# Kernel optimization log

Measured on AMD Instinct MI355X. Metric: run time of the kernel, lower is better.

Reference implementation:

```python
import jax, jax.numpy as jnp
import numpy as np
from jax import lax

IN_CH = 256
NF = 128
B, H, W = 8, 256, 256


def _bn_relu(y, s, b):
    # inference-mode BatchNorm folded into per-channel affine, then ReLU
    return jax.nn.relu(y * s[None, :, None, None] + b[None, :, None, None])


def _upsample_bilinear_ac(x, scale):
    # bilinear upsample, align_corners=True (matches torch nn.Upsample)
    b, c, h, w = x.shape
    Ho, Wo = h * scale, w * scale
    ys = jnp.arange(Ho, dtype=x.dtype) * ((h - 1) / (Ho - 1))
    xs = jnp.arange(Wo, dtype=x.dtype) * ((w - 1) / (Wo - 1))
    y0 = jnp.floor(ys).astype(jnp.int32)
    x0 = jnp.floor(xs).astype(jnp.int32)
    y1 = jnp.minimum(y0 + 1, h - 1)
    x1 = jnp.minimum(x0 + 1, w - 1)
    wy = (ys - y0.astype(x.dtype))[None, None, :, None]
    wx = (xs - x0.astype(x.dtype))[None, None, None, :]
    # interpolate rows then columns
    top = x[:, :, y0, :] * (1 - wy) + x[:, :, y1, :] * wy      # [b,c,Ho,w]
    out = top[:, :, :, x0] * (1 - wx) + top[:, :, :, x1] * wx  # [b,c,Ho,Wo]
    return out


def setup_inputs() -> dict:
    key = jax.random.key(0)
    ks = jax.random.split(key, 6)
    inp = {
        "x": jax.random.normal(ks[0], (B, 64, H, W), dtype=jnp.float32),
        "w1": jax.random.normal(ks[1], (IN_CH, 64, 8, 8), dtype=jnp.float32) * 0.02,
        "bn1_s": jnp.ones((IN_CH,), jnp.float32),
        "bn1_b": jnp.zeros((IN_CH,), jnp.float32),
        "w_fai": jax.random.normal(ks[2], (NF, IN_CH), dtype=jnp.float32) * 0.05,
        "bnf_s": jnp.ones((NF,), jnp.float32),
        "bnf_b": jnp.zeros((NF,), jnp.float32),
        "w_sit": jax.random.normal(ks[3], (NF, IN_CH), dtype=jnp.float32) * 0.05,
        "bns_s": jnp.ones((NF,), jnp.float32),
        "bns_b": jnp.zeros((NF,), jnp.float32),
        "w_gama": jax.random.normal(ks[4], (NF, IN_CH), dtype=jnp.float32) * 0.05,
        "bng_s": jnp.ones((NF,), jnp.float32),
        "bng_b": jnp.zeros((NF,), jnp.float32),
    }
    return inp


def reference(x, w1, bn1_s, bn1_b, w_fai, bnf_s, bnf_b, w_sit, bns_s, bns_b,
              w_gama, bng_s, bng_b):
    # conv1: 8x8 stride-8 conv, BN, ReLU  -> [B, IN_CH, h, w]
    y = lax.conv_general_dilated(x, w1, window_strides=(8, 8), padding="VALID",
                                 dimension_numbers=("NCHW", "OIHW", "NCHW"))
    y = _bn_relu(y, bn1_s, bn1_b)
    b, c, h, w = y.shape
    n = h * w
    # 1x1 conv projections (einsum), BN, ReLU
    fai = _bn_relu(jnp.einsum("bchw,oc->bohw", y, w_fai), bnf_s, bnf_b)
    sit = _bn_relu(jnp.einsum("bchw,oc->bohw", y, w_sit), bns_s, bns_b)
    gama = _bn_relu(jnp.einsum("bchw,oc->bohw", y, w_gama), bng_s, bng_b)
    fai = fai.reshape(b, NF, n)
    sit = sit.reshape(b, NF, n)
    gama = gama.reshape(b, NF, n)
    # non-local attention: sigmoid(fai^T sit) @ gama^T
    sf = jax.nn.sigmoid(jnp.einsum("bcn,bcm->bnm", fai, sit))  # [b, n, n]
    out = jnp.einsum("bnm,bcm->bcn", sf, gama)                  # [b, NF, n]
    out = out.reshape(b, NF, h, w)
    return _upsample_bilinear_ac(out, 8)
```

## Files before the change

kernel.cpp:

```cpp
#include <hip/hip_runtime.h>

typedef __attribute__((ext_vector_type(8))) short short8_t;
typedef __attribute__((ext_vector_type(4))) float float4_t;

__device__ __forceinline__ unsigned short f2bf(float f) {
    unsigned int u = __float_as_uint(f);
    return (unsigned short)((u + 0x7FFFu + ((u >> 16) & 1u)) >> 16);
}
__device__ __forceinline__ unsigned int pkbf(float a, float b) {
    return (unsigned int)f2bf(a) | ((unsigned int)f2bf(b) << 16);
}

__global__ __launch_bounds__(256, 1) void k_conv1(
    const float* __restrict__ x, const float* __restrict__ w1,
    const float* __restrict__ s1, const float* __restrict__ b1,
    unsigned short* __restrict__ y)
{
    __shared__ unsigned short At[128 * 40];
    __shared__ unsigned short Bt[64 * 40];
    const int tid = threadIdx.x;
    const int nt = blockIdx.x, mt = blockIdx.y;
    const int m0 = mt * 128, n0 = nt * 64;
    const int bi = m0 >> 10;
    const int oh0 = (m0 & 1023) >> 5;
    const int lane = tid & 63, wid = tid >> 6;
    const int wm = wid & 1, wn = wid >> 1;
    const int quad = lane >> 4, r16 = lane & 15;
    const int rA = tid >> 4, segA = tid & 15;
    const int ohl = rA >> 2, khl = rA & 3;
    float4_t acc[4][2] = {};

    for (int k0 = 0; k0 < 4096; k0 += 32) {
        const int ic = k0 >> 6;
        const int kh0 = (k0 >> 3) & 7;
        {
            const int xr = (oh0 + ohl) * 8 + kh0 + khl;
            const float* src = x + (((bi * 64 + ic) * 256 + xr) * 256 + segA * 16);
            const float4* s4 = (const float4*)src;
            float4 v0 = s4[0], v1 = s4[1], v2 = s4[2], v3 = s4[3];
            const int dst = (ohl * 32 + segA * 2) * 40 + khl * 8;
            int4 p0, p1;
            p0.x = pkbf(v0.x, v0.y); p0.y = pkbf(v0.z, v0.w);
            p0.z = pkbf(v1.x, v1.y); p0.w = pkbf(v1.z, v1.w);
            p1.x = pkbf(v2.x, v2.y); p1.y = pkbf(v2.z, v2.w);
            p1.z = pkbf(v3.x, v3.y); p1.w = pkbf(v3.z, v3.w);
            *(int4*)&At[dst] = p0;
            *(int4*)&At[dst + 40] = p1;
        }
        #pragma unroll
        for (int j = 0; j < 2; ++j) {
            const int id = j * 256 + tid;
            const int row = id >> 3, p = id & 7;
            float4 v = *(const float4*)(w1 + (n0 + row) * 4096 + k0 + p * 4);
            int2 wv; wv.x = pkbf(v.x, v.y); wv.y = pkbf(v.z, v.w);
            *(int2*)&Bt[row * 40 + p * 4] = wv;
        }
        __syncthreads();
        short8_t aF[4], bF[2];
        #pragma unroll
        for (int i = 0; i < 4; ++i)
            aF[i] = *(const short8_t*)&At[(wm * 64 + i * 16 + r16) * 40 + quad * 8];
        #pragma unroll
        for (int j = 0; j < 2; ++j)
            bF[j] = *(const short8_t*)&Bt[(wn * 32 + j * 16 + r16) * 40 + quad * 8];
        #pragma unroll
        for (int i = 0; i < 4; ++i)
            #pragma unroll
            for (int j = 0; j < 2; ++j)
                acc[i][j] = __builtin_amdgcn_mfma_f32_16x16x32_bf16(aF[i], bF[j], acc[i][j], 0, 0, 0);
        __syncthreads();
    }
    #pragma unroll
    for (int i = 0; i < 4; ++i) {
        const int mg = m0 + wm * 64 + i * 16 + quad * 4;
        #pragma unroll
        for (int j = 0; j < 2; ++j) {
            const int ng = n0 + wn * 32 + j * 16 + r16;
            const float sc = s1[ng], bc = b1[ng];
            #pragma unroll
            for (int r = 0; r < 4; ++r) {
                float v = fmaxf(acc[i][j][r] * sc + bc, 0.f);
                y[(mg + r) * 256 + ng] = f2bf(v);
            }
        }
    }
}

__global__ __launch_bounds__(256, 1) void k_proj(
    const unsigned short* __restrict__ y,
    const float* __restrict__ w_fai, const float* __restrict__ w_sit,
    const float* __restrict__ fs, const float* __restrict__ fb,
    const float* __restrict__ ss, const float* __restrict__ sb,
    unsigned short* __restrict__ P)
{
    __shared__ unsigned short At[128 * 40];
    __shared__ unsigned short Bt[64 * 40];
    const int tid = threadIdx.x;
    const int nt = blockIdx.x, mt = blockIdx.y;
    const int m0 = mt * 128, n0 = nt * 64;
    const float* wsrc = (n0 < 128) ? w_fai : w_sit;
    const float* scs  = (n0 < 128) ? fs : ss;
    const float* bcs  = (n0 < 128) ? fb : sb;
    const int noff = n0 & 127;
    const int lane = tid & 63, wid = tid >> 6;
    const int wm = wid & 1, wn = wid >> 1;
    const int quad = lane >> 4, r16 = lane & 15;
    float4_t acc[4][2] = {};

    for (int k0 = 0; k0 < 256; k0 += 32) {
        #pragma unroll
        for (int j = 0; j < 2; ++j) {
            const int id = j * 256 + tid;
            const int row = id >> 2, p = id & 3;
            int4 v = *(const int4*)(y + (m0 + row) * 256 + k0 + p * 8);
            *(int4*)&At[row * 40 + p * 8] = v;
        }
        #pragma unroll
        for (int j = 0; j < 2; ++j) {
            const int id = j * 256 + tid;
            const int row = id >> 3, p = id & 7;
            float4 v = *(const float4*)(wsrc + (noff + row) * 256 + k0 + p * 4);
            int2 wv; wv.x = pkbf(v.x, v.y); wv.y = pkbf(v.z, v.w);
            *(int2*)&Bt[row * 40 + p * 4] = wv;
        }
        __syncthreads();
        short8_t aF[4], bF[2];
        #pragma unroll
        for (int i = 0; i < 4; ++i)
            aF[i] = *(const short8_t*)&At[(wm * 64 + i * 16 + r16) * 40 + quad * 8];
        #pragma unroll
        for (int j = 0; j < 2; ++j)
            bF[j] = *(const short8_t*)&Bt[(wn * 32 + j * 16 + r16) * 40 + quad * 8];
        #pragma unroll
        for (int i = 0; i < 4; ++i)
            #pragma unroll
            for (int j = 0; j < 2; ++j)
                acc[i][j] = __builtin_amdgcn_mfma_f32_16x16x32_bf16(aF[i], bF[j], acc[i][j], 0, 0, 0);
        __syncthreads();
    }
    #pragma unroll
    for (int i = 0; i < 4; ++i) {
        const int mg = m0 + wm * 64 + i * 16 + quad * 4;
        #pragma unroll
        for (int j = 0; j < 2; ++j) {
            const int ng = n0 + wn * 32 + j * 16 + r16;
            const float sc = scs[ng & 127], bc = bcs[ng & 127];
            #pragma unroll
            for (int r = 0; r < 4; ++r) {
                float v = fmaxf(acc[i][j][r] * sc + bc, 0.f);
                P[(mg + r) * 256 + ng] = f2bf(v);
            }
        }
    }
}

__global__ __launch_bounds__(256, 1) void k_gama(
    const unsigned short* __restrict__ y, const float* __restrict__ wg,
    const float* __restrict__ gs, const float* __restrict__ gb,
    unsigned short* __restrict__ G)
{
    __shared__ unsigned short At[64 * 40];
    __shared__ unsigned short Bt[64 * 40];
    const int tid = threadIdx.x;
    const int nt = blockIdx.x, mt = blockIdx.y;
    const int m0 = mt * 64, n0 = nt * 64;
    const int lane = tid & 63, wid = tid >> 6;
    const int wm = wid & 1, wn = wid >> 1;
    const int quad = lane >> 4, r16 = lane & 15;
    float4_t acc[2][2] = {};

    for (int k0 = 0; k0 < 256; k0 += 32) {
        #pragma unroll
        for (int j = 0; j < 2; ++j) {
            const int id = j * 256 + tid;
            const int row = id >> 3, p = id & 7;
            float4 v = *(const float4*)(wg + (m0 + row) * 256 + k0 + p * 4);
            int2 wv; wv.x = pkbf(v.x, v.y); wv.y = pkbf(v.z, v.w);
            *(int2*)&At[row * 40 + p * 4] = wv;
        }
        {
            const int row = tid >> 2, p = tid & 3;
            int4 v = *(const int4*)(y + (n0 + row) * 256 + k0 + p * 8);
            *(int4*)&Bt[row * 40 + p * 8] = v;
        }
        __syncthreads();
        short8_t aF[2], bF[2];
        #pragma unroll
        for (int i = 0; i < 2; ++i)
            aF[i] = *(const short8_t*)&At[(wm * 32 + i * 16 + r16) * 40 + quad * 8];
        #pragma unroll
        for (int j = 0; j < 2; ++j)
            bF[j] = *(const short8_t*)&Bt[(wn * 32 + j * 16 + r16) * 40 + quad * 8];
        #pragma unroll
        for (int i = 0; i < 2; ++i)
            #pragma unroll
            for (int j = 0; j < 2; ++j)
                acc[i][j] = __builtin_amdgcn_mfma_f32_16x16x32_bf16(aF[i], bF[j], acc[i][j], 0, 0, 0);
        __syncthreads();
    }
    #pragma unroll
    for (int i = 0; i < 2; ++i) {
        const int cbase = m0 + wm * 32 + i * 16 + quad * 4;
        #pragma unroll
        for (int j = 0; j < 2; ++j) {
            const int ngg = n0 + wn * 32 + j * 16 + r16;
            const int nb = ngg >> 10, msp = ngg & 1023;
            #pragma unroll
            for (int r = 0; r < 4; ++r) {
                const int c = cbase + r;
                float v = fmaxf(acc[i][j][r] * gs[c] + gb[c], 0.f);
                G[(nb * 128 + c) * 1024 + msp] = f2bf(v);
            }
        }
    }
}

__global__ __launch_bounds__(256, 1) void k_logits(
    const unsigned short* __restrict__ P, unsigned short* __restrict__ sf)
{
    __shared__ unsigned short At[128 * 40];
    __shared__ unsigned short Bt[64 * 40];
    const int tid = threadIdx.x;
    const int nt = blockIdx.x, mt = blockIdx.y, b = blockIdx.z;
    const int m0 = mt * 128, n0 = nt * 64;
    const int base = b * 1024;
    const int lane = tid & 63, wid = tid >> 6;
    const int wm = wid & 1, wn = wid >> 1;
    const int quad = lane >> 4, r16 = lane & 15;
    float4_t acc[4][2] = {};

    for (int k0 = 0; k0 < 128; k0 += 32) {
        #pragma unroll
        for (int j = 0; j < 2; ++j) {
            const int id = j * 256 + tid;
            const int row = id >> 2, p = id & 3;
            int4 v = *(const int4*)(P + (base + m0 + row) * 256 + k0 + p * 8);
            *(int4*)&At[row * 40 + p * 8] = v;
        }
        {
            const int row = tid >> 2, p = tid & 3;
            int4 v = *(const int4*)(P + (base + n0 + row) * 256 + 128 + k0 + p * 8);
            *(int4*)&Bt[row * 40 + p * 8] = v;
        }
        __syncthreads();
        short8_t aF[4], bF[2];
        #pragma unroll
        for (int i = 0; i < 4; ++i)
            aF[i] = *(const short8_t*)&At[(wm * 64 + i * 16 + r16) * 40 + quad * 8];
        #pragma unroll
        for (int j = 0; j < 2; ++j)
            bF[j] = *(const short8_t*)&Bt[(wn * 32 + j * 16 + r16) * 40 + quad * 8];
        #pragma unroll
        for (int i = 0; i < 4; ++i)
            #pragma unroll
            for (int j = 0; j < 2; ++j)
                acc[i][j] = __builtin_amdgcn_mfma_f32_16x16x32_bf16(aF[i], bF[j], acc[i][j], 0, 0, 0);
        __syncthreads();
    }
    #pragma unroll
    for (int i = 0; i < 4; ++i) {
        const int mg = m0 + wm * 64 + i * 16 + quad * 4;
        #pragma unroll
        for (int j = 0; j < 2; ++j) {
            const int ng = n0 + wn * 32 + j * 16 + r16;
            #pragma unroll
            for (int r = 0; r < 4; ++r) {
                float v = 1.0f / (1.0f + expf(-acc[i][j][r]));
                sf[b * 1048576 + (mg + r) * 1024 + ng] = f2bf(v);
            }
        }
    }
}

__global__ __launch_bounds__(256, 1) void k_av(
    const unsigned short* __restrict__ sf, const unsigned short* __restrict__ G,
    float* __restrict__ O)
{
    __shared__ unsigned short At[64 * 40];
    __shared__ unsigned short Bt[64 * 40];
    const int tid = threadIdx.x;
    const int nt = blockIdx.x, mt = blockIdx.y, b = blockIdx.z;
    const int m0 = mt * 64, n0 = nt * 64;
    const int lane = tid & 63, wid = tid >> 6;
    const int wm = wid & 1, wn = wid >> 1;
    const int quad = lane >> 4, r16 = lane & 15;
    float4_t acc[2][2] = {};

    for (int k0 = 0; k0 < 1024; k0 += 32) {
        {
            const int row = tid >> 2, p = tid & 3;
            int4 v = *(const int4*)(sf + b * 1048576 + (m0 + row) * 1024 + k0 + p * 8);
            *(int4*)&At[row * 40 + p * 8] = v;
            int4 v2 = *(const int4*)(G + (b * 128 + n0 + row) * 1024 + k0 + p * 8);
            *(int4*)&Bt[row * 40 + p * 8] = v2;
        }
        __syncthreads();
        short8_t aF[2], bF[2];
        #pragma unroll
        for (int i = 0; i < 2; ++i)
            aF[i] = *(const short8_t*)&At[(wm * 32 + i * 16 + r16) * 40 + quad * 8];
        #pragma unroll
        for (int j = 0; j < 2; ++j)
            bF[j] = *(const short8_t*)&Bt[(wn * 32 + j * 16 + r16) * 40 + quad * 8];
        #pragma unroll
        for (int i = 0; i < 2; ++i)
            #pragma unroll
            for (int j = 0; j < 2; ++j)
                acc[i][j] = __builtin_amdgcn_mfma_f32_16x16x32_bf16(aF[i], bF[j], acc[i][j], 0, 0, 0);
        __syncthreads();
    }
    #pragma unroll
    for (int i = 0; i < 2; ++i) {
        const int mg = m0 + wm * 32 + i * 16 + quad * 4;
        #pragma unroll
        for (int j = 0; j < 2; ++j) {
            const int ng = n0 + wn * 32 + j * 16 + r16;
            #pragma unroll
            for (int r = 0; r < 4; ++r)
                O[b * 131072 + (mg + r) * 128 + ng] = acc[i][j][r];
        }
    }
}

__global__ __launch_bounds__(256, 1) void k_up(
    const float* __restrict__ O, float* __restrict__ out)
{
    __shared__ float l0[32 * 136];
    __shared__ float l1[32 * 136];
    const int tid = threadIdx.x;
    const int yb = blockIdx.x, b = blockIdx.y;
    const float sc = 31.0f / 255.0f;
    const float fy = yb * sc;
    const int y0 = (int)fy;
    const float wy = fy - (float)y0;
    const int y1 = min(y0 + 1, 31);
    const float4* r0 = (const float4*)(O + b * 131072 + y0 * 4096);
    const float4* r1 = (const float4*)(O + b * 131072 + y1 * 4096);
    #pragma unroll
    for (int j = 0; j < 4; ++j) {
        const int id = j * 256 + tid;
        const int xs = id >> 5, c4 = id & 31;
        *(float4*)(l0 + xs * 136 + c4 * 4) = r0[id];
        *(float4*)(l1 + xs * 136 + c4 * 4) = r1[id];
    }
    __syncthreads();
    const float fx = tid * sc;
    const int x0 = (int)fx;
    const float wx = fx - (float)x0;
    const int x1 = min(x0 + 1, 31);
    const float w00 = (1.f - wy) * (1.f - wx), w01 = (1.f - wy) * wx;
    const float w10 = wy * (1.f - wx), w11 = wy * wx;
    const float* a = l0 + x0 * 136;
    const float* bq = l0 + x1 * 136;
    const float* c = l1 + x0 * 136;
    const float* d = l1 + x1 * 136;
    float* op = out + b * 8388608 + yb * 256 + tid;
    #pragma unroll 4
    for (int ch = 0; ch < 128; ++ch)
        op[ch * 65536] = w00 * a[ch] + w01 * bq[ch] + w10 * c[ch] + w11 * d[ch];
}

extern "C" void kernel_launch(void* const* d_in, const int* in_sizes, int n_in,
                              void* d_out, int out_size, void* d_ws, size_t ws_size,
                              hipStream_t stream) {
    (void)in_sizes; (void)n_in; (void)out_size; (void)ws_size;
    const float* x      = (const float*)d_in[0];
    const float* w1     = (const float*)d_in[1];
    const float* bn1_s  = (const float*)d_in[2];
    const float* bn1_b  = (const float*)d_in[3];
    const float* w_fai  = (const float*)d_in[4];
    const float* bnf_s  = (const float*)d_in[5];
    const float* bnf_b  = (const float*)d_in[6];
    const float* w_sit  = (const float*)d_in[7];
    const float* bns_s  = (const float*)d_in[8];
    const float* bns_b  = (const float*)d_in[9];
    const float* w_gama = (const float*)d_in[10];
    const float* bng_s  = (const float*)d_in[11];
    const float* bng_b  = (const float*)d_in[12];
    float* out = (float*)d_out;

    char* ws = (char*)d_ws;
    unsigned short* y  = (unsigned short*)(ws);
    unsigned short* P  = (unsigned short*)(ws + 4u * 1024 * 1024);
    unsigned short* G  = (unsigned short*)(ws + 8u * 1024 * 1024);
    unsigned short* sf = (unsigned short*)(ws + 10u * 1024 * 1024);
    float*          O  = (float*)(ws + 26u * 1024 * 1024);

    k_conv1 <<<dim3(4, 64),    256, 0, stream>>>(x, w1, bn1_s, bn1_b, y);
    k_proj  <<<dim3(4, 64),    256, 0, stream>>>(y, w_fai, w_sit, bnf_s, bnf_b, bns_s, bns_b, P);
    k_gama  <<<dim3(128, 2),   256, 0, stream>>>(y, w_gama, bng_s, bng_b, G);
    k_logits<<<dim3(16, 8, 8), 256, 0, stream>>>(P, sf);
    k_av    <<<dim3(2, 16, 8), 256, 0, stream>>>(sf, G, O);
    k_up    <<<dim3(256, 8),   256, 0, stream>>>(O, out);
}
```

Baseline: 555.3 us.

## Split-K conv1 and attention-value GEMMs, fuse projections, prefetch conv tiles

Conv1 now covers all 256 output channels per block, splits K four ways across blocks, and prefetches the next tile into registers with a swizzled LDS layout. A new reduce kernel sums the partials and applies BN and ReLU. The three 1x1 projections are merged into one kernel. The attention-value GEMM is split-K by four, and the upsample kernel sums those partials as it loads. The aim is more blocks in flight for the under-filled GEMMs, at the cost of extra partial-sum traffic in global memory and one more launch.

```diff
diff --git a/kernel.cpp b/kernel.cpp
--- a/kernel.cpp
+++ b/kernel.cpp
@@ -11,177 +11,164 @@
     return (unsigned int)f2bf(a) | ((unsigned int)f2bf(b) << 16);
 }
 
-__global__ __launch_bounds__(256, 1) void k_conv1(
+__global__ __launch_bounds__(512, 2) void k_conv1(
     const float* __restrict__ x, const float* __restrict__ w1,
-    const float* __restrict__ s1, const float* __restrict__ b1,
-    unsigned short* __restrict__ y)
+    float* __restrict__ part)
 {
     __shared__ unsigned short At[128 * 40];
-    __shared__ unsigned short Bt[64 * 40];
+    __shared__ unsigned short Bt[256 * 40];
     const int tid = threadIdx.x;
-    const int nt = blockIdx.x, mt = blockIdx.y;
-    const int m0 = mt * 128, n0 = nt * 64;
-    const int bi = m0 >> 10;
-    const int oh0 = (m0 & 1023) >> 5;
+    const int mt = blockIdx.x, kc = blockIdx.y;
+    const int m0 = mt * 128;
+    const int bi = mt >> 3;
+    const int oh0 = (mt & 7) * 4;
     const int lane = tid & 63, wid = tid >> 6;
     const int wm = wid & 1, wn = wid >> 1;
     const int quad = lane >> 4, r16 = lane & 15;
-    const int rA = tid >> 4, segA = tid & 15;
+    const bool isA = tid < 256;
+    const int tA = tid & 255;
+    const int rA = tA >> 4, segA = tA & 15;
     const int ohl = rA >> 2, khl = rA & 3;
-    float4_t acc[4][2] = {};
-
-    for (int k0 = 0; k0 < 4096; k0 += 32) {
-        const int ic = k0 >> 6;
-        const int kh0 = (k0 >> 3) & 7;
-        {
-            const int xr = (oh0 + ohl) * 8 + kh0 + khl;
-            const float* src = x + (((bi * 64 + ic) * 256 + xr) * 256 + segA * 16);
-            const float4* s4 = (const float4*)src;
-            float4 v0 = s4[0], v1 = s4[1], v2 = s4[2], v3 = s4[3];
-            const int dst = (ohl * 32 + segA * 2) * 40 + khl * 8;
+    const int rowA = ohl * 32 + segA * 2;
+    const int koffA = (khl ^ (segA & 3)) * 8;
+    const int kbase = kc * 1024;
+    float4_t acc[4][4] = {};
+    float4 ra[4];
+    float4 rb[8];
+
+    if (isA) {
+        const int ic = kbase >> 6, kh0 = (kbase >> 3) & 7;
+        const int xr = (oh0 + ohl) * 8 + kh0 + khl;
+        const float4* s4 = (const float4*)(x + (((bi * 64 + ic) * 256 + xr) * 256 + segA * 16));
+        ra[0] = s4[0]; ra[1] = s4[1]; ra[2] = s4[2]; ra[3] = s4[3];
+    } else {
+        #pragma unroll
+        for (int l = 0; l < 8; ++l) {
+            const int slot = l * 256 + tA;
+            const int row = slot >> 3, p = slot & 7;
+            rb[l] = *(const float4*)(w1 + row * 4096 + kbase + p * 4);
+        }
+    }
+
+    for (int it = 0; it < 32; ++it) {
+        if (isA) {
             int4 p0, p1;
-            p0.x = pkbf(v0.x, v0.y); p0.y = pkbf(v0.z, v0.w);
-            p0.z = pkbf(v1.x, v1.y); p0.w = pkbf(v1.z, v1.w);
-            p1.x = pkbf(v2.x, v2.y); p1.y = pkbf(v2.z, v2.w);
-            p1.z = pkbf(v3.x, v3.y); p1.w = pkbf(v3.z, v3.w);
-            *(int4*)&At[dst] = p0;
-            *(int4*)&At[dst + 40] = p1;
-        }
-        #pragma unroll
-        for (int j = 0; j < 2; ++j) {
-            const int id = j * 256 + tid;
-            const int row = id >> 3, p = id & 7;
-            float4 v = *(const float4*)(w1 + (n0 + row) * 4096 + k0 + p * 4);
-            int2 wv; wv.x = pkbf(v.x, v.y); wv.y = pkbf(v.z, v.w);
-            *(int2*)&Bt[row * 40 + p * 4] = wv;
-        }
-        __syncthreads();
-        short8_t aF[4], bF[2];
+            p0.x = pkbf(ra[0].x, ra[0].y); p0.y = pkbf(ra[0].z, ra[0].w);
+            p0.z = pkbf(ra[1].x, ra[1].y); p0.w = pkbf(ra[1].z, ra[1].w);
+            p1.x = pkbf(ra[2].x, ra[2].y); p1.y = pkbf(ra[2].z, ra[2].w);
+            p1.z = pkbf(ra[3].x, ra[3].y); p1.w = pkbf(ra[3].z, ra[3].w);
+            *(int4*)&At[rowA * 40 + koffA] = p0;
+            *(int4*)&At[(rowA + 1) * 40 + koffA] = p1;
+        } else {
+            #pragma unroll
+            for (int l = 0; l < 8; ++l) {
+                const int slot = l * 256 + tA;
+                const int row = slot >> 3, p = slot & 7;
+                int2 wv; wv.x = pkbf(rb[l].x, rb[l].y); wv.y = pkbf(rb[l].z, rb[l].w);
+                *(int2*)&Bt[row * 40 + p * 4] = wv;
+            }
+        }
+        __syncthreads();
+        if (it + 1 < 32) {
+            const int k0 = kbase + (it + 1) * 32;
+            if (isA) {
+                const int ic = k0 >> 6, kh0 = (k0 >> 3) & 7;
+                const int xr = (oh0 + ohl) * 8 + kh0 + khl;
+                const float4* s4 = (const float4*)(x + (((bi * 64 + ic) * 256 + xr) * 256 + segA * 16));
+                ra[0] = s4[0]; ra[1] = s4[1]; ra[2] = s4[2]; ra[3] = s4[3];
+            } else {
+                #pragma unroll
+                for (int l = 0; l < 8; ++l) {
+                    const int slot = l * 256 + tA;
+                    const int row = slot >> 3, p = slot & 7;
+                    rb[l] = *(const float4*)(w1 + row * 4096 + k0 + p * 4);
+                }
+            }
+        }
+        short8_t aF[4], bF[4];
+        #pragma unroll
+        for (int i = 0; i < 4; ++i) {
+            const int R = wm * 64 + i * 16 + r16;
+            aF[i] = *(const short8_t*)&At[R * 40 + (quad ^ ((r16 >> 1) & 3)) * 8];
+        }
+        #pragma unroll
+        for (int j = 0; j < 4; ++j)
+            bF[j] = *(const short8_t*)&Bt[(wn * 64 + j * 16 + r16) * 40 + quad * 8];
         #pragma unroll
         for (int i = 0; i < 4; ++i)
-            aF[i] = *(const short8_t*)&At[(wm * 64 + i * 16 + r16) * 40 + quad * 8];
-        #pragma unroll
-        for (int j = 0; j < 2; ++j)
-            bF[j] = *(const short8_t*)&Bt[(wn * 32 + j * 16 + r16) * 40 + quad * 8];
-        #pragma unroll
-        for (int i = 0; i < 4; ++i)
-            #pragma unroll
-            for (int j = 0; j < 2; ++j)
+            #pragma unroll
+            for (int j = 0; j < 4; ++j)
                 acc[i][j] = __builtin_amdgcn_mfma_f32_16x16x32_bf16(aF[i], bF[j], acc[i][j], 0, 0, 0);
         __syncthreads();
     }
+    float* pp = part + ((size_t)kc << 21);
     #pragma unroll
     for (int i = 0; i < 4; ++i) {
         const int mg = m0 + wm * 64 + i * 16 + quad * 4;
         #pragma unroll
-        for (int j = 0; j < 2; ++j) {
-            const int ng = n0 + wn * 32 + j * 16 + r16;
-            const float sc = s1[ng], bc = b1[ng];
-            #pragma unroll
-            for (int r = 0; r < 4; ++r) {
-                float v = fmaxf(acc[i][j][r] * sc + bc, 0.f);
-                y[(mg + r) * 256 + ng] = f2bf(v);
-            }
-        }
-    }
-}
-
-__global__ __launch_bounds__(256, 1) void k_proj(
+        for (int j = 0; j < 4; ++j) {
+            const int ng = wn * 64 + j * 16 + r16;
+            #pragma unroll
+            for (int r = 0; r < 4; ++r)
+                pp[(mg + r) * 256 + ng] = acc[i][j][r];
+        }
+    }
+}
+
+__global__ __launch_bounds__(256, 4) void k_reduce(
+    const float* __restrict__ part, const float* __restrict__ s1,
+    const float* __restrict__ b1, unsigned short* __restrict__ y)
+{
+    const int id = blockIdx.x * 256 + threadIdx.x;
+    const int c4 = id & 63;
+    const float4* p = (const float4*)part + id;
+    float4 a = p[0], b = p[524288], c = p[1048576], d = p[1572864];
+    float4 s = ((const float4*)s1)[c4], bb = ((const float4*)b1)[c4];
+    float vx = fmaxf((a.x + b.x + c.x + d.x) * s.x + bb.x, 0.f);
+    float vy = fmaxf((a.y + b.y + c.y + d.y) * s.y + bb.y, 0.f);
+    float vz = fmaxf((a.z + b.z + c.z + d.z) * s.z + bb.z, 0.f);
+    float vw = fmaxf((a.w + b.w + c.w + d.w) * s.w + bb.w, 0.f);
+    int2 o; o.x = pkbf(vx, vy); o.y = pkbf(vz, vw);
+    ((int2*)y)[id] = o;
+}
+
+__global__ __launch_bounds__(256, 2) void k_proj3(
     const unsigned short* __restrict__ y,
     const float* __restrict__ w_fai, const float* __restrict__ w_sit,
+    const float* __restrict__ w_gama,
     const float* __restrict__ fs, const float* __restrict__ fb,
     const float* __restrict__ ss, const float* __restrict__ sb,
-    unsigned short* __restrict__ P)
-{
-    __shared__ unsigned short At[128 * 40];
-    __shared__ unsigned short Bt[64 * 40];
-    const int tid = threadIdx.x;
-    const int nt = blockIdx.x, mt = blockIdx.y;
-    const int m0 = mt * 128, n0 = nt * 64;
-    const float* wsrc = (n0 < 128) ? w_fai : w_sit;
-    const float* scs  = (n0 < 128) ? fs : ss;
-    const float* bcs  = (n0 < 128) ? fb : sb;
-    const int noff = n0 & 127;
-    const int lane = tid & 63, wid = tid >> 6;
-    const int wm = wid & 1, wn = wid >> 1;
-    const int quad = lane >> 4, r16 = lane & 15;
-    float4_t acc[4][2] = {};
-
-    for (int k0 = 0; k0 < 256; k0 += 32) {
-        #pragma unroll
-        for (int j = 0; j < 2; ++j) {
-            const int id = j * 256 + tid;
-            const int row = id >> 2, p = id & 3;
-            int4 v = *(const int4*)(y + (m0 + row) * 256 + k0 + p * 8);
-            *(int4*)&At[row * 40 + p * 8] = v;
-        }
-        #pragma unroll
-        for (int j = 0; j < 2; ++j) {
-            const int id = j * 256 + tid;
-            const int row = id >> 3, p = id & 7;
-            float4 v = *(const float4*)(wsrc + (noff + row) * 256 + k0 + p * 4);
-            int2 wv; wv.x = pkbf(v.x, v.y); wv.y = pkbf(v.z, v.w);
-            *(int2*)&Bt[row * 40 + p * 4] = wv;
-        }
-        __syncthreads();
-        short8_t aF[4], bF[2];
-        #pragma unroll
-        for (int i = 0; i < 4; ++i)
-            aF[i] = *(const short8_t*)&At[(wm * 64 + i * 16 + r16) * 40 + quad * 8];
-        #pragma unroll
-        for (int j = 0; j < 2; ++j)
-            bF[j] = *(const short8_t*)&Bt[(wn * 32 + j * 16 + r16) * 40 + quad * 8];
-        #pragma unroll
-        for (int i = 0; i < 4; ++i)
-            #pragma unroll
-            for (int j = 0; j < 2; ++j)
-                acc[i][j] = __builtin_amdgcn_mfma_f32_16x16x32_bf16(aF[i], bF[j], acc[i][j], 0, 0, 0);
-        __syncthreads();
-    }
-    #pragma unroll
-    for (int i = 0; i < 4; ++i) {
-        const int mg = m0 + wm * 64 + i * 16 + quad * 4;
-        #pragma unroll
-        for (int j = 0; j < 2; ++j) {
-            const int ng = n0 + wn * 32 + j * 16 + r16;
-            const float sc = scs[ng & 127], bc = bcs[ng & 127];
-            #pragma unroll
-            for (int r = 0; r < 4; ++r) {
-                float v = fmaxf(acc[i][j][r] * sc + bc, 0.f);
-                P[(mg + r) * 256 + ng] = f2bf(v);
-            }
-        }
-    }
-}
-
-__global__ __launch_bounds__(256, 1) void k_gama(
-    const unsigned short* __restrict__ y, const float* __restrict__ wg,
     const float* __restrict__ gs, const float* __restrict__ gb,
-    unsigned short* __restrict__ G)
+    unsigned short* __restrict__ P, unsigned short* __restrict__ G)
 {
     __shared__ unsigned short At[64 * 40];
     __shared__ unsigned short Bt[64 * 40];
     const int tid = threadIdx.x;
     const int nt = blockIdx.x, mt = blockIdx.y;
-    const int m0 = mt * 64, n0 = nt * 64;
+    const int m0 = mt * 64;
+    const float *W, *S, *Bb;
+    if (nt < 2)      { W = w_fai;  S = fs; Bb = fb; }
+    else if (nt < 4) { W = w_sit;  S = ss; Bb = sb; }
+    else             { W = w_gama; S = gs; Bb = gb; }
+    const int roff = (nt * 64) & 127;
     const int lane = tid & 63, wid = tid >> 6;
     const int wm = wid & 1, wn = wid >> 1;
     const int quad = lane >> 4, r16 = lane & 15;
     float4_t acc[2][2] = {};
 
     for (int k0 = 0; k0 < 256; k0 += 32) {
-        #pragma unroll
-        for (int j = 0; j < 2; ++j) {
-            const int id = j * 256 + tid;
-            const int row = id >> 3, p = id & 7;
-            float4 v = *(const float4*)(wg + (m0 + row) * 256 + k0 + p * 4);
+        {
+            const int row = tid >> 2, pp = tid & 3;
+            *(int4*)&At[row * 40 + pp * 8] =
+                *(const int4*)(y + (m0 + row) * 256 + k0 + pp * 8);
+        }
+        #pragma unroll
+        for (int l = 0; l < 2; ++l) {
+            const int slot = l * 256 + tid;
+            const int row = slot >> 3, pp = slot & 7;
+            float4 v = *(const float4*)(W + (roff + row) * 256 + k0 + pp * 4);
             int2 wv; wv.x = pkbf(v.x, v.y); wv.y = pkbf(v.z, v.w);
-            *(int2*)&At[row * 40 + p * 4] = wv;
-        }
-        {
-            const int row = tid >> 2, p = tid & 3;
-            int4 v = *(const int4*)(y + (n0 + row) * 256 + k0 + p * 8);
-            *(int4*)&Bt[row * 40 + p * 8] = v;
+            *(int2*)&Bt[row * 40 + pp * 4] = wv;
         }
         __syncthreads();
         short8_t aF[2], bF[2];
@@ -200,22 +187,32 @@
     }
     #pragma unroll
     for (int i = 0; i < 2; ++i) {
-        const int cbase = m0 + wm * 32 + i * 16 + quad * 4;
+        const int mg = m0 + wm * 32 + i * 16 + quad * 4;
         #pragma unroll
         for (int j = 0; j < 2; ++j) {
-            const int ngg = n0 + wn * 32 + j * 16 + r16;
-            const int nb = ngg >> 10, msp = ngg & 1023;
-            #pragma unroll
-            for (int r = 0; r < 4; ++r) {
-                const int c = cbase + r;
-                float v = fmaxf(acc[i][j][r] * gs[c] + gb[c], 0.f);
-                G[(nb * 128 + c) * 1024 + msp] = f2bf(v);
+            const int nl = wn * 32 + j * 16 + r16;
+            const float sc = S[roff + nl], bc = Bb[roff + nl];
+            if (nt < 4) {
+                const int col = nt * 64 + nl;
+                #pragma unroll
+                for (int r = 0; r < 4; ++r) {
+                    float v = fmaxf(acc[i][j][r] * sc + bc, 0.f);
+                    P[(mg + r) * 256 + col] = f2bf(v);
+                }
+            } else {
+                const int c = roff + nl;
+                #pragma unroll
+                for (int r = 0; r < 4; ++r) {
+                    float v = fmaxf(acc[i][j][r] * sc + bc, 0.f);
+                    const int sp = mg + r;
+                    G[((sp >> 10) * 128 + c) * 1024 + (sp & 1023)] = f2bf(v);
+                }
             }
         }
     }
 }
 
-__global__ __launch_bounds__(256, 1) void k_logits(
+__global__ __launch_bounds__(256, 2) void k_logits(
     const unsigned short* __restrict__ P, unsigned short* __restrict__ sf)
 {
     __shared__ unsigned short At[128 * 40];
@@ -234,13 +231,13 @@
         for (int j = 0; j < 2; ++j) {
             const int id = j * 256 + tid;
             const int row = id >> 2, p = id & 3;
-            int4 v = *(const int4*)(P + (base + m0 + row) * 256 + k0 + p * 8);
-            *(int4*)&At[row * 40 + p * 8] = v;
+            *(int4*)&At[row * 40 + p * 8] =
+                *(const int4*)(P + (base + m0 + row) * 256 + k0 + p * 8);
         }
         {
             const int row = tid >> 2, p = tid & 3;
-            int4 v = *(const int4*)(P + (base + n0 + row) * 256 + 128 + k0 + p * 8);
-            *(int4*)&Bt[row * 40 + p * 8] = v;
+            *(int4*)&Bt[row * 40 + p * 8] =
+                *(const int4*)(P + (base + n0 + row) * 256 + 128 + k0 + p * 8);
         }
         __syncthreads();
         short8_t aF[4], bF[2];
@@ -272,58 +269,66 @@
     }
 }
 
-__global__ __launch_bounds__(256, 1) void k_av(
+__global__ __launch_bounds__(256, 2) void k_av(
     const unsigned short* __restrict__ sf, const unsigned short* __restrict__ G,
-    float* __restrict__ O)
+    float* __restrict__ Opart)
 {
     __shared__ unsigned short At[64 * 40];
-    __shared__ unsigned short Bt[64 * 40];
+    __shared__ unsigned short Bt[128 * 40];
     const int tid = threadIdx.x;
-    const int nt = blockIdx.x, mt = blockIdx.y, b = blockIdx.z;
-    const int m0 = mt * 64, n0 = nt * 64;
+    const int mt = blockIdx.x, zz = blockIdx.y;
+    const int b = zz >> 2, kc = zz & 3;
+    const int m0 = mt * 64;
     const int lane = tid & 63, wid = tid >> 6;
     const int wm = wid & 1, wn = wid >> 1;
     const int quad = lane >> 4, r16 = lane & 15;
-    float4_t acc[2][2] = {};
-
-    for (int k0 = 0; k0 < 1024; k0 += 32) {
+    float4_t acc[2][4] = {};
+
+    for (int it = 0; it < 8; ++it) {
+        const int k0 = kc * 256 + it * 32;
         {
             const int row = tid >> 2, p = tid & 3;
-            int4 v = *(const int4*)(sf + b * 1048576 + (m0 + row) * 1024 + k0 + p * 8);
-            *(int4*)&At[row * 40 + p * 8] = v;
-            int4 v2 = *(const int4*)(G + (b * 128 + n0 + row) * 1024 + k0 + p * 8);
-            *(int4*)&Bt[row * 40 + p * 8] = v2;
-        }
-        __syncthreads();
-        short8_t aF[2], bF[2];
+            *(int4*)&At[row * 40 + p * 8] =
+                *(const int4*)(sf + b * 1048576 + (m0 + row) * 1024 + k0 + p * 8);
+        }
+        #pragma unroll
+        for (int l = 0; l < 2; ++l) {
+            const int slot = l * 256 + tid;
+            const int row = slot >> 2, p = slot & 3;
+            *(int4*)&Bt[row * 40 + p * 8] =
+                *(const int4*)(G + (b * 128 + row) * 1024 + k0 + p * 8);
+        }
+        __syncthreads();
+        short8_t aF[2], bF[4];
         #pragma unroll
         for (int i = 0; i < 2; ++i)
             aF[i] = *(const short8_t*)&At[(wm * 32 + i * 16 + r16) * 40 + quad * 8];
         #pragma unroll
-        for (int j = 0; j < 2; ++j)
-            bF[j] = *(const short8_t*)&Bt[(wn * 32 + j * 16 + r16) * 40 + quad * 8];
+        for (int j = 0; j < 4; ++j)
+            bF[j] = *(const short8_t*)&Bt[(wn * 64 + j * 16 + r16) * 40 + quad * 8];
         #pragma unroll
         for (int i = 0; i < 2; ++i)
             #pragma unroll
-            for (int j = 0; j < 2; ++j)
+            for (int j = 0; j < 4; ++j)
                 acc[i][j] = __builtin_amdgcn_mfma_f32_16x16x32_bf16(aF[i], bF[j], acc[i][j], 0, 0, 0);
         __syncthreads();
     }
+    float* op = Opart + (size_t)kc * 1048576 + (size_t)b * 131072;
     #pragma unroll
     for (int i = 0; i < 2; ++i) {
         const int mg = m0 + wm * 32 + i * 16 + quad * 4;
         #pragma unroll
-        for (int j = 0; j < 2; ++j) {
-            const int ng = n0 + wn * 32 + j * 16 + r16;
+        for (int j = 0; j < 4; ++j) {
+            const int ng = wn * 64 + j * 16 + r16;
             #pragma unroll
             for (int r = 0; r < 4; ++r)
-                O[b * 131072 + (mg + r) * 128 + ng] = acc[i][j][r];
-        }
-    }
-}
-
-__global__ __launch_bounds__(256, 1) void k_up(
-    const float* __restrict__ O, float* __restrict__ out)
+                op[(mg + r) * 128 + ng] = acc[i][j][r];
+        }
+    }
+}
+
+__global__ __launch_bounds__(256, 2) void k_up(
+    const float* __restrict__ Opart, float* __restrict__ out)
 {
     __shared__ float l0[32 * 136];
     __shared__ float l1[32 * 136];
@@ -333,28 +338,35 @@
     const float fy = yb * sc;
     const int y0 = (int)fy;
     const float wy = fy - (float)y0;
-    const int y1 = min(y0 + 1, 31);
-    const float4* r0 = (const float4*)(O + b * 131072 + y0 * 4096);
-    const float4* r1 = (const float4*)(O + b * 131072 + y1 * 4096);
+    const int y1 = (y0 + 1 < 32) ? y0 + 1 : 31;
+    const float4* r0 = (const float4*)(Opart + (size_t)b * 131072 + y0 * 4096);
+    const float4* r1 = (const float4*)(Opart + (size_t)b * 131072 + y1 * 4096);
     #pragma unroll
     for (int j = 0; j < 4; ++j) {
         const int id = j * 256 + tid;
         const int xs = id >> 5, c4 = id & 31;
-        *(float4*)(l0 + xs * 136 + c4 * 4) = r0[id];
-        *(float4*)(l1 + xs * 136 + c4 * 4) = r1[id];
+        float4 a0 = r0[id], a1 = r1[id];
+        #pragma unroll
+        for (int kc = 1; kc < 4; ++kc) {
+            float4 t0 = r0[id + kc * 262144], t1 = r1[id + kc * 262144];
+            a0.x += t0.x; a0.y += t0.y; a0.z += t0.z; a0.w += t0.w;
+            a1.x += t1.x; a1.y += t1.y; a1.z += t1.z; a1.w += t1.w;
+        }
+        *(float4*)(l0 + xs * 136 + c4 * 4) = a0;
+        *(float4*)(l1 + xs * 136 + c4 * 4) = a1;
     }
     __syncthreads();
     const float fx = tid * sc;
     const int x0 = (int)fx;
     const float wx = fx - (float)x0;
-    const int x1 = min(x0 + 1, 31);
+    const int x1 = (x0 + 1 < 32) ? x0 + 1 : 31;
     const float w00 = (1.f - wy) * (1.f - wx), w01 = (1.f - wy) * wx;
     const float w10 = wy * (1.f - wx), w11 = wy * wx;
     const float* a = l0 + x0 * 136;
     const float* bq = l0 + x1 * 136;
     const float* c = l1 + x0 * 136;
     const float* d = l1 + x1 * 136;
-    float* op = out + b * 8388608 + yb * 256 + tid;
+    float* op = out + (size_t)b * 8388608 + yb * 256 + tid;
     #pragma unroll 4
     for (int ch = 0; ch < 128; ++ch)
         op[ch * 65536] = w00 * a[ch] + w01 * bq[ch] + w10 * c[ch] + w11 * d[ch];
@@ -380,16 +392,19 @@
     float* out = (float*)d_out;
 
     char* ws = (char*)d_ws;
-    unsigned short* y  = (unsigned short*)(ws);
-    unsigned short* P  = (unsigned short*)(ws + 4u * 1024 * 1024);
-    unsigned short* G  = (unsigned short*)(ws + 8u * 1024 * 1024);
-    unsigned short* sf = (unsigned short*)(ws + 10u * 1024 * 1024);
-    float*          O  = (float*)(ws + 26u * 1024 * 1024);
-
-    k_conv1 <<<dim3(4, 64),    256, 0, stream>>>(x, w1, bn1_s, bn1_b, y);
-    k_proj  <<<dim3(4, 64),    256, 0, stream>>>(y, w_fai, w_sit, bnf_s, bnf_b, bns_s, bns_b, P);
-    k_gama  <<<dim3(128, 2),   256, 0, stream>>>(y, w_gama, bng_s, bng_b, G);
+    float*          pc    = (float*)ws;
+    unsigned short* sf    = (unsigned short*)ws;
+    float*          Opart = (float*)(ws + 16u * 1024 * 1024);
+    unsigned short* y     = (unsigned short*)(ws + 32u * 1024 * 1024);
+    unsigned short* P     = (unsigned short*)(ws + 36u * 1024 * 1024);
+    unsigned short* G     = (unsigned short*)(ws + 40u * 1024 * 1024);
+
+    k_conv1 <<<dim3(64, 4),    512, 0, stream>>>(x, w1, pc);
+    k_reduce<<<dim3(2048),     256, 0, stream>>>(pc, bn1_s, bn1_b, y);
+    k_proj3 <<<dim3(6, 128),   256, 0, stream>>>(y, w_fai, w_sit, w_gama,
+                                                 bnf_s, bnf_b, bns_s, bns_b,
+                                                 bng_s, bng_b, P, G);
     k_logits<<<dim3(16, 8, 8), 256, 0, stream>>>(P, sf);
-    k_av    <<<dim3(2, 16, 8), 256, 0, stream>>>(sf, G, O);
-    k_up    <<<dim3(256, 8),   256, 0, stream>>>(O, out);
-}
+    k_av    <<<dim3(16, 32),   256, 0, stream>>>(sf, G, Opart);
+    k_up    <<<dim3(256, 8),   256, 0, stream>>>(Opart, out);
+}
```

Result: faster. 494.0 us (-11.0%).
